# Optimization experiments

Hardware: AMD Instinct MI355X
Metric: run time of the kernel (lower is better)

Reference implementation:

```python
import jax, jax.numpy as jnp
import numpy as np

N = 8192
F_IN = 128
F_OUT = 128
NEG_SLOPE = 0.2


def setup_inputs() -> dict:
    key = jax.random.key(0)
    k_h, k_adj, k_W, k_a = jax.random.split(key, 4)
    h = jax.random.normal(k_h, (N, F_IN), dtype=jnp.float32)
    # binary adjacency mask as float (the module multiplies scores by adj)
    adj = (jax.random.uniform(k_adj, (N, N)) < 0.05).astype(jnp.float32)
    # nn.Linear(in, out, bias=False): weight shape [out, in]
    W = jax.random.normal(k_W, (F_OUT, F_IN), dtype=jnp.float32) / np.sqrt(F_IN)
    # nn.Linear(2*out, 1, bias=False): weight shape [1, 2*out]
    a = jax.random.normal(k_a, (1, 2 * F_OUT), dtype=jnp.float32) / np.sqrt(2 * F_OUT)
    return {"h": h, "adj": adj, "W": W, "a": a}


def reference(h, adj, W, a):
    # Wh: [N, F_out]
    Wh = h @ W.T
    f = Wh.shape[-1]
    # a([Wh_i ; Wh_j]) factored: e[i, j] = leaky_relu(Wh[i]@a1 + Wh[j]@a2)
    a1 = a[0, :f]  # [F_out]
    a2 = a[0, f:]  # [F_out]
    s_i = Wh @ a1  # [N]
    s_j = Wh @ a2  # [N]
    e = jax.nn.leaky_relu(s_i[:, None] + s_j[None, :], NEG_SLOPE)  # [N, N]
    # faithful to original: softmax over dim=1 of e * adj (multiplicative mask)
    attention = jax.nn.softmax(e * adj, axis=1)  # [N, N]
    return attention @ Wh  # [N, F_out]
```

## Files before the change

kernel.cpp:

```cpp
#include <hip/hip_runtime.h>

#define N_NODES 8192
#define FDIM 128
#define NEG_SLOPE 0.2f
#define SEG 512

__device__ inline unsigned fkey(float x) {
  unsigned b = __float_as_uint(x);
  return (b & 0x80000000u) ? ~b : (b | 0x80000000u);
}

__global__ __launch_bounds__(256) void wh_fused_kernel(
    const float* __restrict__ h, const float* __restrict__ W,
    const float* __restrict__ a, float* __restrict__ Wh,
    float* __restrict__ s1g, float* __restrict__ s2g,
    float* __restrict__ S, unsigned* __restrict__ s2max_key) {
  __shared__ float Wt[FDIM * 132];
  __shared__ float rows[32 * 132];
  const int t = threadIdx.x;
  const int base = blockIdx.x * 32;
  for (int it = 0; it < 64; ++it) {
    int idx = t + 256 * it;
    int o = idx >> 7, k = idx & 127;
    Wt[k * 132 + o] = W[idx];
  }
  for (int it = 0; it < 16; ++it) {
    int idx = t + 256 * it;
    int r = idx >> 7, col = idx & 127;
    rows[r * 132 + col] = h[(size_t)base * FDIM + idx];
  }
  __syncthreads();
  const int c4 = (t & 31) * 4;
  const int g = t >> 5;
  float acc[4][4];
#pragma unroll
  for (int rr = 0; rr < 4; ++rr)
#pragma unroll
    for (int cc = 0; cc < 4; ++cc) acc[rr][cc] = 0.f;
  for (int k = 0; k < FDIM; ++k) {
    float4 wv = *(const float4*)&Wt[k * 132 + c4];
    float rv[4];
#pragma unroll
    for (int rr = 0; rr < 4; ++rr) rv[rr] = rows[(4 * g + rr) * 132 + k];
#pragma unroll
    for (int rr = 0; rr < 4; ++rr) {
      acc[rr][0] += rv[rr] * wv.x;
      acc[rr][1] += rv[rr] * wv.y;
      acc[rr][2] += rv[rr] * wv.z;
      acc[rr][3] += rv[rr] * wv.w;
    }
  }
#pragma unroll
  for (int rr = 0; rr < 4; ++rr) {
    int r = base + 4 * g + rr;
    *(float4*)&Wh[(size_t)r * FDIM + c4] =
        make_float4(acc[rr][0], acc[rr][1], acc[rr][2], acc[rr][3]);
  }
  {
    float4 a1c = *(const float4*)&a[c4];
    float4 a2c = *(const float4*)&a[FDIM + c4];
    float p1[4], p2[4];
#pragma unroll
    for (int rr = 0; rr < 4; ++rr) {
      p1[rr] = acc[rr][0] * a1c.x + acc[rr][1] * a1c.y +
               acc[rr][2] * a1c.z + acc[rr][3] * a1c.w;
      p2[rr] = acc[rr][0] * a2c.x + acc[rr][1] * a2c.y +
               acc[rr][2] * a2c.z + acc[rr][3] * a2c.w;
    }
#pragma unroll
    for (int rr = 0; rr < 4; ++rr)
      for (int off = 16; off; off >>= 1) {
        p1[rr] += __shfl_down(p1[rr], off, 32);
        p2[rr] += __shfl_down(p2[rr], off, 32);
      }
    if ((t & 31) == 0) {
      unsigned kmax = 0;
#pragma unroll
      for (int rr = 0; rr < 4; ++rr) {
        int r = base + 4 * g + rr;
        s1g[r] = p1[rr];
        s2g[r] = p2[rr];
        unsigned kk = fkey(p2[rr]);
        kmax = kk > kmax ? kk : kmax;
      }
      atomicMax(s2max_key, kmax);
    }
  }
  __syncthreads();
  float4 cs = make_float4(acc[0][0] + acc[1][0] + acc[2][0] + acc[3][0],
                          acc[0][1] + acc[1][1] + acc[2][1] + acc[3][1],
                          acc[0][2] + acc[1][2] + acc[2][2] + acc[3][2],
                          acc[0][3] + acc[1][3] + acc[2][3] + acc[3][3]);
  *(float4*)&rows[g * FDIM + c4] = cs;
  __syncthreads();
  if (t < FDIM) {
    float s = 0.f;
#pragma unroll
    for (int gg = 0; gg < 8; ++gg) s += rows[gg * FDIM + t];
    atomicAdd(&S[t], s);
  }
}

__global__ __launch_bounds__(256) void gat_row_kernel(
    const float* __restrict__ adj, const float* __restrict__ Wh,
    const float* __restrict__ s1, const float* __restrict__ s2,
    const unsigned* __restrict__ s2max_key, const float* __restrict__ S,
    float* __restrict__ out) {
  const int i = blockIdx.x;
  const int t = threadIdx.x;
  const int lane = t & 63;
  const int wave = t >> 6;
  __shared__ float2 pairs[4 * SEG];
  __shared__ int counts[4];
  __shared__ float red2[4];
  __shared__ float fpart[4][FDIM];

  const float s1i = s1[i];
  unsigned kk = *s2max_key;
  unsigned bb = (kk & 0x80000000u) ? (kk ^ 0x80000000u) : ~kk;
  float pm = s1i + __uint_as_float(bb);
  pm = pm > 0.f ? pm : NEG_SLOPE * pm;
  const float m = fmaxf(pm, 0.f);
  const float em = __expf(-m);

  const float4* __restrict__ arow = (const float4*)(adj + (size_t)i * N_NODES);
  const float4* __restrict__ s2v = (const float4*)s2;
  float2* __restrict__ mypairs = pairs + wave * SEG;
  const unsigned long long lmask = (1ull << lane) - 1ull;
  const int half = lane >> 5, lq = lane & 31;
  const float4* __restrict__ Wh4 = (const float4*)Wh;

  int cbase = 0, drained = 0;
  float lsum = 0.f;
  float ax = 0.f, ay = 0.f, az = 0.f, aw = 0.f;

  float4 av = arow[t], sv = s2v[t];
#pragma unroll
  for (int it = 0; it < 8; ++it) {
    float4 avn, svn;
    if (it < 7) {
      avn = arow[(it + 1) * 256 + t];
      svn = s2v[(it + 1) * 256 + t];
    }
    const int j4 = it * 256 + t;
    float vv[4] = {av.x, av.y, av.z, av.w};
    float ss[4] = {sv.x, sv.y, sv.z, sv.w};
#pragma unroll
    for (int c = 0; c < 4; ++c) {
      bool pred = (vv[c] != 0.f);
      float e = s1i + ss[c];
      e = e > 0.f ? e : NEG_SLOPE * e;
      float p = __expf(e - m);
      unsigned long long b = __ballot(pred);
      if (pred) {
        int pos = cbase + (int)__popcll(b & lmask);
        if (pos < SEG)
          mypairs[pos] = make_float2(p - em, __int_as_float(j4 * 4 + c));
      }
      lsum += pred ? p : 0.f;
      cbase += (int)__popcll(b);
    }
    av = avn; sv = svn;
    int cc = cbase < SEG ? cbase : SEG;
    while (drained + 8 <= cc) {
      float2 pr0 = mypairs[drained + half];
      float2 pr1 = mypairs[drained + 2 + half];
      float2 pr2 = mypairs[drained + 4 + half];
      float2 pr3 = mypairs[drained + 6 + half];
      float4 v0 = Wh4[((size_t)__float_as_int(pr0.y) << 5) + lq];
      float4 v1 = Wh4[((size_t)__float_as_int(pr1.y) << 5) + lq];
      float4 v2 = Wh4[((size_t)__float_as_int(pr2.y) << 5) + lq];
      float4 v3 = Wh4[((size_t)__float_as_int(pr3.y) << 5) + lq];
      ax += pr0.x * v0.x + pr1.x * v1.x + pr2.x * v2.x + pr3.x * v3.x;
      ay += pr0.x * v0.y + pr1.x * v1.y + pr2.x * v2.y + pr3.x * v3.y;
      az += pr0.x * v0.z + pr1.x * v1.z + pr2.x * v2.z + pr3.x * v3.z;
      aw += pr0.x * v0.w + pr1.x * v1.w + pr2.x * v2.w + pr3.x * v3.w;
      drained += 8;
    }
  }
  {
    int cc = cbase < SEG ? cbase : SEG;
    while (drained < cc) {
      int p0 = drained + half;
      bool ok = p0 < cc;
      float2 pr = mypairs[ok ? p0 : 0];
      float4 v = Wh4[((size_t)__float_as_int(pr.y) << 5) + lq];
      float w = ok ? pr.x : 0.f;
      ax += w * v.x; ay += w * v.y; az += w * v.z; aw += w * v.w;
      drained += 2;
    }
  }
  ax += __shfl_down(ax, 32);
  ay += __shfl_down(ay, 32);
  az += __shfl_down(az, 32);
  aw += __shfl_down(aw, 32);
  for (int off = 32; off; off >>= 1) lsum += __shfl_down(lsum, off);
  if (lane == 0) {
    red2[wave] = lsum;
    counts[wave] = cbase < SEG ? cbase : SEG;
  }
  if (lane < 32)
    *(float4*)&fpart[wave][4 * lq] = make_float4(ax, ay, az, aw);
  __syncthreads();
  if (t < FDIM) {
    int cnt = counts[0] + counts[1] + counts[2] + counts[3];
    float l = red2[0] + red2[1] + red2[2] + red2[3]
              + (float)(N_NODES - cnt) * em;
    float o = (fpart[0][t] + fpart[1][t] + fpart[2][t] + fpart[3][t]
               + em * S[t]) / l;
    out[(size_t)i * FDIM + t] = o;
  }
}

extern "C" void kernel_launch(void* const* d_in, const int* in_sizes, int n_in,
                              void* d_out, int out_size, void* d_ws, size_t ws_size,
                              hipStream_t stream) {
  const float* h   = (const float*)d_in[0];
  const float* adj = (const float*)d_in[1];
  const float* W   = (const float*)d_in[2];
  const float* a   = (const float*)d_in[3];
  float* out = (float*)d_out;
  float* Wh = (float*)d_ws;
  float* s1 = Wh + (size_t)N_NODES * FDIM;
  float* s2 = s1 + N_NODES;
  float* S  = s2 + N_NODES;
  unsigned* s2max_key = (unsigned*)(S + FDIM);

  hipMemsetAsync(S, 0, FDIM * sizeof(float) + sizeof(unsigned), stream);
  hipLaunchKernelGGL(wh_fused_kernel, dim3(N_NODES / 32), dim3(256), 0, stream,
                     h, W, a, Wh, s1, s2, S, s2max_key);
  hipLaunchKernelGGL(gat_row_kernel, dim3(N_NODES), dim3(256), 0, stream,
                     adj, Wh, s1, s2, s2max_key, S, out);
}
```

Measured before the change: 464.2 us.

## Replace sparse gather aggregation with dense bf16 MFMA attention matmul

The per-row sparse gather over compacted neighbor lists is replaced by a dense attention-times-Wh product on MFMA 32x32x16 bf16 instructions. Wh is split into high and low bf16 parts for extra precision and stored pre-swizzled in fragment layout. Exponentials are factored into per-row and per-column terms, so each probability becomes a select and a multiply. K is split across two blocks that combine through atomics, and a separate normalization kernel follows. The intent is to trade the irregular gather for regular streaming and matrix-core compute, at the cost of bf16 rounding of the probabilities and a larger memset.

Measured after the change: 481.4 us. 3.7% more time.

```diff
diff --git a/kernel.cpp b/kernel.cpp
--- a/kernel.cpp
+++ b/kernel.cpp
@@ -3,26 +3,38 @@
 #define N_NODES 8192
 #define FDIM 128
 #define NEG_SLOPE 0.2f
-#define SEG 512
+
+typedef short short8 __attribute__((ext_vector_type(8)));
+typedef float floatx16 __attribute__((ext_vector_type(16)));
 
 __device__ inline unsigned fkey(float x) {
   unsigned b = __float_as_uint(x);
   return (b & 0x80000000u) ? ~b : (b | 0x80000000u);
 }
+__device__ inline float fkey_dec(unsigned kk) {
+  unsigned bb = (kk & 0x80000000u) ? (kk ^ 0x80000000u) : ~kk;
+  return __uint_as_float(bb);
+}
+__device__ inline unsigned short bf16_rn(float x) {
+  unsigned u = __float_as_uint(x);
+  u += 0x7fffu + ((u >> 16) & 1u);
+  return (unsigned short)(u >> 16);
+}
 
 __global__ __launch_bounds__(256) void wh_fused_kernel(
     const float* __restrict__ h, const float* __restrict__ W,
-    const float* __restrict__ a, float* __restrict__ Wh,
-    float* __restrict__ s1g, float* __restrict__ s2g,
-    float* __restrict__ S, unsigned* __restrict__ s2max_key) {
-  __shared__ float Wt[FDIM * 132];
+    const float* __restrict__ a, float* __restrict__ s1g,
+    float* __restrict__ Bj, float* __restrict__ Dj,
+    unsigned* __restrict__ s2max_key,
+    unsigned short* __restrict__ Bfh, unsigned short* __restrict__ Bfl) {
+  __shared__ float Wt[FDIM * 129];
   __shared__ float rows[32 * 132];
   const int t = threadIdx.x;
   const int base = blockIdx.x * 32;
   for (int it = 0; it < 64; ++it) {
     int idx = t + 256 * it;
     int o = idx >> 7, k = idx & 127;
-    Wt[k * 132 + o] = W[idx];
+    Wt[k * 129 + o] = W[idx];
   }
   for (int it = 0; it < 16; ++it) {
     int idx = t + 256 * it;
@@ -38,7 +50,7 @@
 #pragma unroll
     for (int cc = 0; cc < 4; ++cc) acc[rr][cc] = 0.f;
   for (int k = 0; k < FDIM; ++k) {
-    float4 wv = *(const float4*)&Wt[k * 132 + c4];
+    float4 wv = *(const float4*)&Wt[k * 129 + c4];
     float rv[4];
 #pragma unroll
     for (int rr = 0; rr < 4; ++rr) rv[rr] = rows[(4 * g + rr) * 132 + k];
@@ -49,12 +61,6 @@
       acc[rr][2] += rv[rr] * wv.z;
       acc[rr][3] += rv[rr] * wv.w;
     }
-  }
-#pragma unroll
-  for (int rr = 0; rr < 4; ++rr) {
-    int r = base + 4 * g + rr;
-    *(float4*)&Wh[(size_t)r * FDIM + c4] =
-        make_float4(acc[rr][0], acc[rr][1], acc[rr][2], acc[rr][3]);
   }
   {
     float4 a1c = *(const float4*)&a[c4];
@@ -79,7 +85,8 @@
       for (int rr = 0; rr < 4; ++rr) {
         int r = base + 4 * g + rr;
         s1g[r] = p1[rr];
-        s2g[r] = p2[rr];
+        Bj[r] = __expf(p2[rr]);
+        Dj[r] = __expf(NEG_SLOPE * p2[rr]);
         unsigned kk = fkey(p2[rr]);
         kmax = kk > kmax ? kk : kmax;
       }
@@ -87,129 +94,144 @@
     }
   }
   __syncthreads();
-  float4 cs = make_float4(acc[0][0] + acc[1][0] + acc[2][0] + acc[3][0],
-                          acc[0][1] + acc[1][1] + acc[2][1] + acc[3][1],
-                          acc[0][2] + acc[1][2] + acc[2][2] + acc[3][2],
-                          acc[0][3] + acc[1][3] + acc[2][3] + acc[3][3]);
-  *(float4*)&rows[g * FDIM + c4] = cs;
-  __syncthreads();
-  if (t < FDIM) {
-    float s = 0.f;
-#pragma unroll
-    for (int gg = 0; gg < 8; ++gg) s += rows[gg * FDIM + t];
-    atomicAdd(&S[t], s);
-  }
-}
-
-__global__ __launch_bounds__(256) void gat_row_kernel(
-    const float* __restrict__ adj, const float* __restrict__ Wh,
-    const float* __restrict__ s1, const float* __restrict__ s2,
-    const unsigned* __restrict__ s2max_key, const float* __restrict__ S,
-    float* __restrict__ out) {
-  const int i = blockIdx.x;
+  unsigned short* hbuf = (unsigned short*)Wt;
+  unsigned short* lbuf = hbuf + 4096;
+#pragma unroll
+  for (int rr = 0; rr < 4; ++rr)
+#pragma unroll
+    for (int cc = 0; cc < 4; ++cc) {
+      float x = acc[rr][cc];
+      unsigned short hb = bf16_rn(x);
+      float hf = __uint_as_float(((unsigned)hb) << 16);
+      unsigned short lb = bf16_rn(x - hf);
+      int lr = 4 * g + rr;
+      int n = c4 + cc;
+      int idx = (((lr >> 4) * 4 + (n >> 5)) * 64 + ((lr >> 3) & 1) * 32 +
+                 (n & 31)) * 8 + (lr & 7);
+      hbuf[idx] = hb;
+      lbuf[idx] = lb;
+    }
+  __syncthreads();
+  {
+    const unsigned* hsrc = (const unsigned*)hbuf;
+    const unsigned* lsrc = (const unsigned*)lbuf;
+    unsigned* hdst = (unsigned*)(Bfh + (size_t)base * FDIM);
+    unsigned* ldst = (unsigned*)(Bfl + (size_t)base * FDIM);
+    for (int q = t; q < 2048; q += 256) { hdst[q] = hsrc[q]; ldst[q] = lsrc[q]; }
+  }
+}
+
+__global__ __launch_bounds__(256) void gat_mfma_kernel(
+    const float* __restrict__ adj,
+    const unsigned short* __restrict__ Bfh,
+    const unsigned short* __restrict__ Bfl,
+    const float* __restrict__ s1g, const float* __restrict__ Bj,
+    const float* __restrict__ Dj, const unsigned* __restrict__ s2max_key,
+    float* __restrict__ num, float* __restrict__ l_ws) {
+  __shared__ float cred[4 * 32 * FDIM];
   const int t = threadIdx.x;
   const int lane = t & 63;
   const int wave = t >> 6;
-  __shared__ float2 pairs[4 * SEG];
-  __shared__ int counts[4];
-  __shared__ float red2[4];
-  __shared__ float fpart[4][FDIM];
-
-  const float s1i = s1[i];
-  unsigned kk = *s2max_key;
-  unsigned bb = (kk & 0x80000000u) ? (kk ^ 0x80000000u) : ~kk;
-  float pm = s1i + __uint_as_float(bb);
-  pm = pm > 0.f ? pm : NEG_SLOPE * pm;
-  const float m = fmaxf(pm, 0.f);
+  const int rowgrp = blockIdx.x >> 1;
+  const int ksplit = blockIdx.x & 1;
+  const int hh = lane >> 5;
+  const int m0 = rowgrp * 32 + (lane & 31);
+  const int kbase = ksplit * 4096 + wave * 1024;
+
+  const float s1i = s1g[m0];
+  float pmv = s1i + fkey_dec(*s2max_key);
+  pmv = pmv > 0.f ? pmv : NEG_SLOPE * pmv;
+  const float m = fmaxf(pmv, 0.f);
+  const float Ai = __expf(s1i - m);
+  const float Ci = __expf(NEG_SLOPE * s1i - m);
+  const float Ti = __expf(-s1i);
   const float em = __expf(-m);
 
-  const float4* __restrict__ arow = (const float4*)(adj + (size_t)i * N_NODES);
-  const float4* __restrict__ s2v = (const float4*)s2;
-  float2* __restrict__ mypairs = pairs + wave * SEG;
-  const unsigned long long lmask = (1ull << lane) - 1ull;
-  const int half = lane >> 5, lq = lane & 31;
-  const float4* __restrict__ Wh4 = (const float4*)Wh;
-
-  int cbase = 0, drained = 0;
-  float lsum = 0.f;
-  float ax = 0.f, ay = 0.f, az = 0.f, aw = 0.f;
-
-  float4 av = arow[t], sv = s2v[t];
-#pragma unroll
-  for (int it = 0; it < 8; ++it) {
-    float4 avn, svn;
-    if (it < 7) {
-      avn = arow[(it + 1) * 256 + t];
-      svn = s2v[(it + 1) * 256 + t];
-    }
-    const int j4 = it * 256 + t;
-    float vv[4] = {av.x, av.y, av.z, av.w};
-    float ss[4] = {sv.x, sv.y, sv.z, sv.w};
-#pragma unroll
-    for (int c = 0; c < 4; ++c) {
-      bool pred = (vv[c] != 0.f);
-      float e = s1i + ss[c];
-      e = e > 0.f ? e : NEG_SLOPE * e;
-      float p = __expf(e - m);
-      unsigned long long b = __ballot(pred);
-      if (pred) {
-        int pos = cbase + (int)__popcll(b & lmask);
-        if (pos < SEG)
-          mypairs[pos] = make_float2(p - em, __int_as_float(j4 * 4 + c));
-      }
-      lsum += pred ? p : 0.f;
-      cbase += (int)__popcll(b);
-    }
-    av = avn; sv = svn;
-    int cc = cbase < SEG ? cbase : SEG;
-    while (drained + 8 <= cc) {
-      float2 pr0 = mypairs[drained + half];
-      float2 pr1 = mypairs[drained + 2 + half];
-      float2 pr2 = mypairs[drained + 4 + half];
-      float2 pr3 = mypairs[drained + 6 + half];
-      float4 v0 = Wh4[((size_t)__float_as_int(pr0.y) << 5) + lq];
-      float4 v1 = Wh4[((size_t)__float_as_int(pr1.y) << 5) + lq];
-      float4 v2 = Wh4[((size_t)__float_as_int(pr2.y) << 5) + lq];
-      float4 v3 = Wh4[((size_t)__float_as_int(pr3.y) << 5) + lq];
-      ax += pr0.x * v0.x + pr1.x * v1.x + pr2.x * v2.x + pr3.x * v3.x;
-      ay += pr0.x * v0.y + pr1.x * v1.y + pr2.x * v2.y + pr3.x * v3.y;
-      az += pr0.x * v0.z + pr1.x * v1.z + pr2.x * v2.z + pr3.x * v3.z;
-      aw += pr0.x * v0.w + pr1.x * v1.w + pr2.x * v2.w + pr3.x * v3.w;
-      drained += 8;
-    }
-  }
-  {
-    int cc = cbase < SEG ? cbase : SEG;
-    while (drained < cc) {
-      int p0 = drained + half;
-      bool ok = p0 < cc;
-      float2 pr = mypairs[ok ? p0 : 0];
-      float4 v = Wh4[((size_t)__float_as_int(pr.y) << 5) + lq];
-      float w = ok ? pr.x : 0.f;
-      ax += w * v.x; ay += w * v.y; az += w * v.z; aw += w * v.w;
-      drained += 2;
-    }
-  }
-  ax += __shfl_down(ax, 32);
-  ay += __shfl_down(ay, 32);
-  az += __shfl_down(az, 32);
-  aw += __shfl_down(aw, 32);
-  for (int off = 32; off; off >>= 1) lsum += __shfl_down(lsum, off);
-  if (lane == 0) {
-    red2[wave] = lsum;
-    counts[wave] = cbase < SEG ? cbase : SEG;
-  }
-  if (lane < 32)
-    *(float4*)&fpart[wave][4 * lq] = make_float4(ax, ay, az, aw);
-  __syncthreads();
-  if (t < FDIM) {
-    int cnt = counts[0] + counts[1] + counts[2] + counts[3];
-    float l = red2[0] + red2[1] + red2[2] + red2[3]
-              + (float)(N_NODES - cnt) * em;
-    float o = (fpart[0][t] + fpart[1][t] + fpart[2][t] + fpart[3][t]
-               + em * S[t]) / l;
-    out[(size_t)i * FDIM + t] = o;
-  }
+  const float* adj_lane = adj + (size_t)m0 * N_NODES + hh * 8;
+  const float* bj_lane = Bj + hh * 8;
+  const float* dj_lane = Dj + hh * 8;
+  const short8* BH = (const short8*)Bfh;
+  const short8* BL = (const short8*)Bfl;
+
+  floatx16 acc0, acc1, acc2, acc3;
+#pragma unroll
+  for (int i = 0; i < 16; ++i) { acc0[i] = 0.f; acc1[i] = 0.f; acc2[i] = 0.f; acc3[i] = 0.f; }
+  float rsum = 0.f;
+
+#pragma unroll 2
+  for (int k = kbase; k < kbase + 1024; k += 16) {
+    float4 a0 = *(const float4*)(adj_lane + k);
+    float4 a1 = *(const float4*)(adj_lane + k + 4);
+    float4 b0 = *(const float4*)(bj_lane + k);
+    float4 b1 = *(const float4*)(bj_lane + k + 4);
+    float4 d0 = *(const float4*)(dj_lane + k);
+    float4 d1 = *(const float4*)(dj_lane + k + 4);
+    size_t fb = ((size_t)(k >> 4) * 4) * 64 + lane;
+    short8 bh0 = BH[fb],       bl0 = BL[fb];
+    short8 bh1 = BH[fb + 64],  bl1 = BL[fb + 64];
+    short8 bh2 = BH[fb + 128], bl2 = BL[fb + 128];
+    short8 bh3 = BH[fb + 192], bl3 = BL[fb + 192];
+
+    float av[8] = {a0.x, a0.y, a0.z, a0.w, a1.x, a1.y, a1.z, a1.w};
+    float bv[8] = {b0.x, b0.y, b0.z, b0.w, b1.x, b1.y, b1.z, b1.w};
+    float dv[8] = {d0.x, d0.y, d0.z, d0.w, d1.x, d1.y, d1.z, d1.w};
+    float pv[8];
+#pragma unroll
+    for (int e = 0; e < 8; ++e) {
+      bool cpos = bv[e] > Ti;
+      float p = (cpos ? Ai : Ci) * (cpos ? bv[e] : dv[e]);
+      p = (av[e] != 0.f) ? p : em;
+      pv[e] = p;
+      rsum += p;
+    }
+    union { uint4 u; short8 s; } pk;
+    pk.u.x = (unsigned)bf16_rn(pv[0]) | ((unsigned)bf16_rn(pv[1]) << 16);
+    pk.u.y = (unsigned)bf16_rn(pv[2]) | ((unsigned)bf16_rn(pv[3]) << 16);
+    pk.u.z = (unsigned)bf16_rn(pv[4]) | ((unsigned)bf16_rn(pv[5]) << 16);
+    pk.u.w = (unsigned)bf16_rn(pv[6]) | ((unsigned)bf16_rn(pv[7]) << 16);
+    short8 af = pk.s;
+
+    acc0 = __builtin_amdgcn_mfma_f32_32x32x16_bf16(af, bh0, acc0, 0, 0, 0);
+    acc0 = __builtin_amdgcn_mfma_f32_32x32x16_bf16(af, bl0, acc0, 0, 0, 0);
+    acc1 = __builtin_amdgcn_mfma_f32_32x32x16_bf16(af, bh1, acc1, 0, 0, 0);
+    acc1 = __builtin_amdgcn_mfma_f32_32x32x16_bf16(af, bl1, acc1, 0, 0, 0);
+    acc2 = __builtin_amdgcn_mfma_f32_32x32x16_bf16(af, bh2, acc2, 0, 0, 0);
+    acc2 = __builtin_amdgcn_mfma_f32_32x32x16_bf16(af, bl2, acc2, 0, 0, 0);
+    acc3 = __builtin_amdgcn_mfma_f32_32x32x16_bf16(af, bh3, acc3, 0, 0, 0);
+    acc3 = __builtin_amdgcn_mfma_f32_32x32x16_bf16(af, bl3, acc3, 0, 0, 0);
+  }
+
+  rsum += __shfl_xor(rsum, 32);
+  if (lane < 32) atomicAdd(&l_ws[rowgrp * 32 + lane], rsum);
+
+#pragma unroll
+  for (int reg = 0; reg < 16; ++reg) {
+    int r = (reg & 3) + 8 * (reg >> 2) + 4 * hh;
+    int cbase = (wave * 32 + r) * FDIM + (lane & 31);
+    cred[cbase]      = acc0[reg];
+    cred[cbase + 32] = acc1[reg];
+    cred[cbase + 64] = acc2[reg];
+    cred[cbase + 96] = acc3[reg];
+  }
+  __syncthreads();
+#pragma unroll
+  for (int q = 0; q < 16; ++q) {
+    int idx = q * 256 + t;
+    int r = idx >> 7, c = idx & 127;
+    float s = cred[r * FDIM + c] + cred[(32 + r) * FDIM + c] +
+              cred[(64 + r) * FDIM + c] + cred[(96 + r) * FDIM + c];
+    atomicAdd(&num[(size_t)(rowgrp * 32 + r) * FDIM + c], s);
+  }
+}
+
+__global__ __launch_bounds__(256) void norm_kernel(
+    const float* __restrict__ num, const float* __restrict__ l_ws,
+    float* __restrict__ out) {
+  int idx = blockIdx.x * 256 + threadIdx.x;
+  float4 v = ((const float4*)num)[idx];
+  float li = l_ws[idx >> 5];
+  ((float4*)out)[idx] =
+      make_float4(v.x / li, v.y / li, v.z / li, v.w / li);
 }
 
 extern "C" void kernel_launch(void* const* d_in, const int* in_sizes, int n_in,
@@ -220,15 +242,21 @@
   const float* W   = (const float*)d_in[2];
   const float* a   = (const float*)d_in[3];
   float* out = (float*)d_out;
-  float* Wh = (float*)d_ws;
-  float* s1 = Wh + (size_t)N_NODES * FDIM;
-  float* s2 = s1 + N_NODES;
-  float* S  = s2 + N_NODES;
-  unsigned* s2max_key = (unsigned*)(S + FDIM);
-
-  hipMemsetAsync(S, 0, FDIM * sizeof(float) + sizeof(unsigned), stream);
+  float* num = (float*)d_ws;
+  float* l_ws = num + (size_t)N_NODES * FDIM;
+  unsigned* key = (unsigned*)(l_ws + N_NODES);
+  float* s1 = (float*)(key + 1);
+  float* Bj = s1 + N_NODES;
+  float* Dj = Bj + N_NODES;
+  unsigned short* Bfh = (unsigned short*)(Dj + N_NODES);
+  unsigned short* Bfl = Bfh + (size_t)N_NODES * FDIM;
+
+  hipMemsetAsync(num, 0, ((size_t)N_NODES * FDIM + N_NODES + 1) * sizeof(float),
+                 stream);
   hipLaunchKernelGGL(wh_fused_kernel, dim3(N_NODES / 32), dim3(256), 0, stream,
-                     h, W, a, Wh, s1, s2, S, s2max_key);
-  hipLaunchKernelGGL(gat_row_kernel, dim3(N_NODES), dim3(256), 0, stream,
-                     adj, Wh, s1, s2, s2max_key, S, out);
-}
+                     h, W, a, s1, Bj, Dj, key, Bfh, Bfl);
+  hipLaunchKernelGGL(gat_mfma_kernel, dim3(512), dim3(256), 0, stream,
+                     adj, Bfh, Bfl, s1, Bj, Dj, key, num, l_ws);
+  hipLaunchKernelGGL(norm_kernel, dim3(N_NODES * FDIM / 4 / 256), dim3(256), 0,
+                     stream, num, l_ws, out);
+}
```
